# Optimization experiments

Hardware: AMD Instinct MI355X
Metric: run time of the kernel (lower is better)

Reference implementation:

```python
import jax, jax.numpy as jnp
import numpy as np

TOP_K = 2  # num_experts_per_tok


def setup_inputs() -> dict:
    key = jax.random.key(0)
    ks = jax.random.split(key, 5)
    B, T, D, E, F = 2, 2048, 1024, 8, 2048
    scale_d = 1.0 / np.sqrt(D)
    scale_f = 1.0 / np.sqrt(F)
    return {
        "x": jax.random.normal(ks[0], (B, T, D), jnp.float32),
        "kernel_router_DE": jax.random.normal(ks[1], (D, E), jnp.float32) * scale_d,
        "kernel_gating_EDF": jax.random.normal(ks[2], (E, D, F), jnp.float32) * scale_d,
        "kernel_up_EDF": jax.random.normal(ks[3], (E, D, F), jnp.float32) * scale_d,
        "kernel_down_EFD": jax.random.normal(ks[4], (E, F, D), jnp.float32) * scale_f,
    }


def reference(x, kernel_router_DE, kernel_gating_EDF, kernel_up_EDF, kernel_down_EFD):
    E = kernel_router_DE.shape[-1]
    x = x.astype(jnp.float32)

    # --- Router: logits -> softmax -> top_k -> renormalize with softmax ---
    router_logits_BTE = jnp.einsum('BTD,DE->BTE', x, kernel_router_DE)
    probs_BTE = jax.nn.softmax(router_logits_BTE.astype(jnp.float32), axis=-1)
    weights_BTX, indices_BTX = jax.lax.top_k(probs_BTE, TOP_K)
    norm_weights_BTX = jax.nn.softmax(weights_BTX, axis=-1)

    # --- Scatter top-k weights back to dense per-expert weights ---
    one_hot_BTXE = jax.nn.one_hot(indices_BTX, num_classes=E, dtype=jnp.float32)
    full_weights_BTE = jnp.sum(one_hot_BTXE * norm_weights_BTX[..., None], axis=2)

    # --- Dense all-expert MLP (gating * up -> down), weighted combine ---
    gating_BTEF = jnp.einsum('BTD,EDF->BTEF', x, kernel_gating_EDF)
    fuse_BTEF = jax.nn.silu(gating_BTEF) * jnp.einsum('BTD,EDF->BTEF', x, kernel_up_EDF)
    down_BTED = jnp.einsum('BTEF,EFD->BTED', fuse_BTEF, kernel_down_EFD)
    out_BTD = jnp.einsum('BTED,BTE->BTD', down_BTED, full_weights_BTE)
    return out_BTD.astype(jnp.float32)
```

## Files before the change

### kernel.cpp

```cpp
#include <hip/hip_runtime.h>
#include <cstdint>

#define N_TOK 4096
#define DIM   1024
#define NEXP  8
#define FDIM  2048

typedef _Float16 f16_t;
typedef _Float16 f16x8 __attribute__((ext_vector_type(8)));
typedef float    f32x4 __attribute__((ext_vector_type(4)));

__device__ inline unsigned packh(float a, float b) {
    union { f16_t h[2]; unsigned u; } p;
    p.h[0] = (f16_t)a; p.h[1] = (f16_t)b;
    return p.u;
}

__device__ inline void gl2lds16(const void* g, void* l) {
    __builtin_amdgcn_global_load_lds(
        (const __attribute__((address_space(1))) unsigned*)g,
        (__attribute__((address_space(3))) unsigned*)l, 16, 0, 0);
}

__device__ void transpose_tile(const float* __restrict__ in, f16_t* __restrict__ out,
                               int R, int C, int tiles_r, int tix, unsigned (*sP)[68])
{
    int rb = (tix % tiles_r) * 128;
    int cb = (tix / tiles_r) * 64;
    int t = threadIdx.x;
    int dp = t >> 2;
    int fc = (t & 3) * 16;
    const float* r0 = in + (size_t)(rb + 2 * dp) * C + cb + fc;
    const float* r1 = r0 + C;
#pragma unroll
    for (int j = 0; j < 16; j += 4) {
        float4 a = *(const float4*)(r0 + j);
        float4 b = *(const float4*)(r1 + j);
        sP[fc + j + 0][dp] = packh(a.x, b.x);
        sP[fc + j + 1][dp] = packh(a.y, b.y);
        sP[fc + j + 2][dp] = packh(a.z, b.z);
        sP[fc + j + 3][dp] = packh(a.w, b.w);
    }
    __syncthreads();
    int c = t >> 2;
    int rc = t & 3;
    uint4* dst = (uint4*)(out + (size_t)(cb + c) * R + rb + rc * 32);
    const unsigned* src = &sP[c][rc * 16];
#pragma unroll
    for (int j = 0; j < 4; j++)
        dst[j] = *(const uint4*)(src + j * 4);
}

__global__ __launch_bounds__(256) void prep_kernel(
    const float* __restrict__ x, const float* __restrict__ wr,
    const float* __restrict__ wg, const float* __restrict__ wu, const float* __restrict__ wd,
    f16_t* __restrict__ xf, f16_t* __restrict__ wgT, f16_t* __restrict__ wuT, f16_t* __restrict__ wdT,
    float* __restrict__ topw, int* __restrict__ counts, int* __restrict__ bucket)
{
    __shared__ union { float r[NEXP][DIM]; unsigned sP[64][68]; } sh;
    __shared__ int sIdx[32];
    int bx = blockIdx.x;
    int tid = threadIdx.x;

    if (bx >= 256) {
        if (bx < 256 + 4096) {
            int tix = bx - 256;
            int m = tix >> 8;
            int tt = tix & 255;
            const float* in = (m < 8) ? wg + (size_t)m * DIM * FDIM : wu + (size_t)(m - 8) * DIM * FDIM;
            f16_t* out      = (m < 8) ? wgT + (size_t)m * DIM * FDIM : wuT + (size_t)(m - 8) * DIM * FDIM;
            transpose_tile(in, out, DIM, FDIM, DIM / 128, tt, sh.sP);
        } else {
            int tix = bx - (256 + 4096);
            int m = tix >> 8;
            int tt = tix & 255;
            transpose_tile(wd + (size_t)m * FDIM * DIM, wdT + (size_t)m * FDIM * DIM,
                           FDIM, DIM, FDIM / 128, tt, sh.sP);
        }
        return;
    }

    for (int i = tid; i < DIM * NEXP / 4; i += 256) {
        float4 v = ((const float4*)wr)[i];
        int base = i * 4;
        sh.r[(base + 0) & 7][(base + 0) >> 3] = v.x;
        sh.r[(base + 1) & 7][(base + 1) >> 3] = v.y;
        sh.r[(base + 2) & 7][(base + 2) >> 3] = v.z;
        sh.r[(base + 3) & 7][(base + 3) >> 3] = v.w;
    }
    __syncthreads();
    int wave = tid >> 6, lane = tid & 63;
    int t0 = bx * 16 + wave * 4;
    for (int tt = 0; tt < 4; ++tt) {
        int t = t0 + tt;
        float acc[NEXP];
#pragma unroll
        for (int e = 0; e < NEXP; e++) acc[e] = 0.f;
        const float* xr = x + (size_t)t * DIM;
        f16_t* xo = xf + (size_t)t * DIM;
#pragma unroll
        for (int k = 0; k < DIM / 64; k++) {
            int d = lane + k * 64;
            float xv = xr[d];
            xo[d] = (f16_t)xv;
#pragma unroll
            for (int e = 0; e < NEXP; e++) acc[e] += xv * sh.r[e][d];
        }
#pragma unroll
        for (int e = 0; e < NEXP; e++) {
#pragma unroll
            for (int off = 32; off > 0; off >>= 1)
                acc[e] += __shfl_xor(acc[e], off, 64);
        }
        if (lane == 0) {
            float mx = acc[0];
#pragma unroll
            for (int e = 1; e < NEXP; e++) mx = fmaxf(mx, acc[e]);
            float p[NEXP]; float s = 0.f;
#pragma unroll
            for (int e = 0; e < NEXP; e++) { p[e] = expf(acc[e] - mx); s += p[e]; }
            float inv = 1.f / s;
#pragma unroll
            for (int e = 0; e < NEXP; e++) p[e] *= inv;
            int i1 = 0; float p1 = p[0];
#pragma unroll
            for (int e = 1; e < NEXP; e++) if (p[e] > p1) { p1 = p[e]; i1 = e; }
            int i2 = -1; float p2 = -1.f;
#pragma unroll
            for (int e = 0; e < NEXP; e++) if (e != i1 && p[e] > p2) { p2 = p[e]; i2 = e; }
            float e2 = expf(p2 - p1);
            float w1 = 1.f / (1.f + e2);
            topw[t * 2 + 0] = w1;
            topw[t * 2 + 1] = e2 * w1;
            int j = (wave * 4 + tt) * 2;
            sIdx[j + 0] = i1;
            sIdx[j + 1] = i2;
        }
    }
    __syncthreads();
    if (tid < NEXP) {
        int cnt = 0;
#pragma unroll
        for (int j = 0; j < 32; j++) cnt += (sIdx[j] == tid) ? 1 : 0;
        if (cnt > 0) {
            int pos = atomicAdd(&counts[tid * 32], cnt);
#pragma unroll
            for (int j = 0; j < 32; j++)
                if (sIdx[j] == tid)
                    bucket[tid * N_TOK + pos++] = (bx * 16 + (j >> 1)) * 2 + (j & 1);
        }
    }
}

__global__ __launch_bounds__(256) void transpose_d_kernel(
    const float* __restrict__ wd, f16_t* __restrict__ wdT)
{
    __shared__ unsigned sP[64][68];
    int m = blockIdx.x >> 8;
    int tt = blockIdx.x & 255;
    transpose_tile(wd + (size_t)m * FDIM * DIM, wdT + (size_t)m * FDIM * DIM,
                   FDIM, DIM, FDIM / 128, tt, sP);
}

__global__ __launch_bounds__(256) void gateup_kernel(
    const f16_t* __restrict__ xf,
    const f16_t* __restrict__ wgT, const f16_t* __restrict__ wuT,
    const int* __restrict__ counts, const int* __restrict__ bucket,
    const float* __restrict__ topw, f16_t* __restrict__ H)
{
    int e = blockIdx.z;
    int cnt = counts[e * 32];
    int m0 = blockIdx.y * 128;
    if (m0 >= cnt) return;
    int n0 = blockIdx.x * 64;

    __shared__ f16_t sA[128 * 32];
    __shared__ f16_t sBg[64 * 32];
    __shared__ f16_t sBu[64 * 32];
    __shared__ int sEnt[128];

    int tid = threadIdx.x;
    if (tid < 128) {
        int i = m0 + tid;
        sEnt[tid] = bucket[e * N_TOK + (i < cnt ? i : m0)];
    }
    __syncthreads();

    int wave = tid >> 6, lane = tid & 63;
    int q = ((lane & 3) - (lane >> 3)) & 3;
    int rA0 = wave * 32 + (lane >> 2);
    int rA1 = rA0 + 16;
    int rB  = wave * 16 + (lane >> 2);
    const f16_t* gA0 = xf + (size_t)(sEnt[rA0] >> 1) * DIM + q * 8;
    const f16_t* gA1 = xf + (size_t)(sEnt[rA1] >> 1) * DIM + q * 8;
    const f16_t* gBg = wgT + ((size_t)e * FDIM + n0 + rB) * DIM + q * 8;
    const f16_t* gBu = wuT + ((size_t)e * FDIM + n0 + rB) * DIM + q * 8;
    f16_t* lA0 = &sA[wave * 1024 + lane * 8];
    f16_t* lA1 = lA0 + 512;
    f16_t* lBg = &sBg[wave * 512 + lane * 8];
    f16_t* lBu = &sBu[wave * 512 + lane * 8];

    f32x4 accG[4][2], accU[4][2];
    f32x4 zero = {0.f, 0.f, 0.f, 0.f};
#pragma unroll
    for (int i = 0; i < 4; i++)
#pragma unroll
        for (int j = 0; j < 2; j++) { accG[i][j] = zero; accU[i][j] = zero; }

    int wm = (wave & 1) * 64, wn = (wave >> 1) * 32;
    int fm = lane & 15, quad = lane >> 4;
    int p8 = ((quad + (fm >> 1)) & 3) * 8;

    for (int k0 = 0; k0 < DIM; k0 += 32) {
        gl2lds16(gA0 + k0, lA0);
        gl2lds16(gA1 + k0, lA1);
        gl2lds16(gBg + k0, lBg);
        gl2lds16(gBu + k0, lBu);
        __syncthreads();
        f16x8 af[4], bg[2], bu[2];
#pragma unroll
        for (int mi = 0; mi < 4; mi++)
            af[mi] = *(const f16x8*)&sA[(wm + mi * 16 + fm) * 32 + p8];
#pragma unroll
        for (int ni = 0; ni < 2; ni++) {
            bg[ni] = *(const f16x8*)&sBg[(wn + ni * 16 + fm) * 32 + p8];
            bu[ni] = *(const f16x8*)&sBu[(wn + ni * 16 + fm) * 32 + p8];
        }
#pragma unroll
        for (int mi = 0; mi < 4; mi++)
#pragma unroll
            for (int ni = 0; ni < 2; ni++) {
                accG[mi][ni] = __builtin_amdgcn_mfma_f32_16x16x32_f16(af[mi], bg[ni], accG[mi][ni], 0, 0, 0);
                accU[mi][ni] = __builtin_amdgcn_mfma_f32_16x16x32_f16(af[mi], bu[ni], accU[mi][ni], 0, 0, 0);
            }
        __syncthreads();
    }
    int crow = quad * 4, ccol = fm;
#pragma unroll
    for (int mi = 0; mi < 4; mi++) {
#pragma unroll
        for (int i = 0; i < 4; i++) {
            int m = wm + mi * 16 + crow + i;
            if (m0 + m < cnt) {
                int ent = sEnt[m];
                float w = topw[ent];
                f16_t* hr = H + (size_t)ent * FDIM + n0 + wn;
#pragma unroll
                for (int ni = 0; ni < 2; ni++) {
                    float g = accG[mi][ni][i], u = accU[mi][ni][i];
                    float h = (g / (1.f + __expf(-g))) * u * w;
                    hr[ni * 16 + ccol] = (f16_t)h;
                }
            }
        }
    }
}

__global__ __launch_bounds__(256) void down_kernel(
    const f16_t* __restrict__ H, const f16_t* __restrict__ wdT,
    const int* __restrict__ counts, const int* __restrict__ bucket,
    float* __restrict__ Y)
{
    int e = blockIdx.z;
    int cnt = counts[e * 32];
    int m0 = blockIdx.y * 128;
    if (m0 >= cnt) return;
    int n0 = blockIdx.x * 128;

    __shared__ f16_t sA[128 * 32];
    __shared__ f16_t sB[128 * 32];
    __shared__ int sEnt[128];

    int tid = threadIdx.x;
    if (tid < 128) {
        int i = m0 + tid;
        sEnt[tid] = bucket[e * N_TOK + (i < cnt ? i : m0)];
    }
    __syncthreads();

    int wave = tid >> 6, lane = tid & 63;
    int q = ((lane & 3) - (lane >> 3)) & 3;
    int r0 = wave * 32 + (lane >> 2);
    int r1 = r0 + 16;
    const f16_t* gA0 = H + (size_t)sEnt[r0] * FDIM + q * 8;
    const f16_t* gA1 = H + (size_t)sEnt[r1] * FDIM + q * 8;
    const f16_t* gB0 = wdT + ((size_t)e * DIM + n0 + r0) * FDIM + q * 8;
    const f16_t* gB1 = wdT + ((size_t)e * DIM + n0 + r1) * FDIM + q * 8;
    f16_t* lA0 = &sA[wave * 1024 + lane * 8];
    f16_t* lA1 = lA0 + 512;
    f16_t* lB0 = &sB[wave * 1024 + lane * 8];
    f16_t* lB1 = lB0 + 512;

    f32x4 acc[4][4];
    f32x4 zero = {0.f, 0.f, 0.f, 0.f};
#pragma unroll
    for (int i = 0; i < 4; i++)
#pragma unroll
        for (int j = 0; j < 4; j++) acc[i][j] = zero;

    int wm = (wave & 1) * 64, wn = (wave >> 1) * 64;
    int fm = lane & 15, quad = lane >> 4;
    int p8 = ((quad + (fm >> 1)) & 3) * 8;

    for (int k0 = 0; k0 < FDIM; k0 += 32) {
        gl2lds16(gA0 + k0, lA0);
        gl2lds16(gA1 + k0, lA1);
        gl2lds16(gB0 + k0, lB0);
        gl2lds16(gB1 + k0, lB1);
        __syncthreads();
        f16x8 af[4], bf[4];
#pragma unroll
        for (int mi = 0; mi < 4; mi++)
            af[mi] = *(const f16x8*)&sA[(wm + mi * 16 + fm) * 32 + p8];
#pragma unroll
        for (int ni = 0; ni < 4; ni++)
            bf[ni] = *(const f16x8*)&sB[(wn + ni * 16 + fm) * 32 + p8];
#pragma unroll
        for (int mi = 0; mi < 4; mi++)
#pragma unroll
            for (int ni = 0; ni < 4; ni++)
                acc[mi][ni] = __builtin_amdgcn_mfma_f32_16x16x32_f16(af[mi], bf[ni], acc[mi][ni], 0, 0, 0);
        __syncthreads();
    }
    int crow = quad * 4, ccol = fm;
#pragma unroll
    for (int mi = 0; mi < 4; mi++) {
#pragma unroll
        for (int i = 0; i < 4; i++) {
            int m = wm + mi * 16 + crow + i;
            if (m0 + m < cnt) {
                int ent = sEnt[m];
                float* yr = Y + (size_t)ent * DIM + n0 + wn;
#pragma unroll
                for (int ni = 0; ni < 4; ni++)
                    yr[ni * 16 + ccol] = acc[mi][ni][i];
            }
        }
    }
}

__global__ __launch_bounds__(256) void combine_kernel(
    const float* __restrict__ Y, float* __restrict__ out)
{
    int i = blockIdx.x * 256 + threadIdx.x;
    int t = i >> 8;
    int c = i & 255;
    float4 a = ((const float4*)Y)[(size_t)(2 * t) * 256 + c];
    float4 b = ((const float4*)Y)[(size_t)(2 * t + 1) * 256 + c];
    float4 o;
    o.x = a.x + b.x; o.y = a.y + b.y; o.z = a.z + b.z; o.w = a.w + b.w;
    ((float4*)out)[i] = o;
}

extern "C" void kernel_launch(void* const* d_in, const int* in_sizes, int n_in,
                              void* d_out, int out_size, void* d_ws, size_t ws_size,
                              hipStream_t stream) {
    const float* x  = (const float*)d_in[0];
    const float* wr = (const float*)d_in[1];
    const float* wg = (const float*)d_in[2];
    const float* wu = (const float*)d_in[3];
    const float* wd = (const float*)d_in[4];
    float* out = (float*)d_out;
    char* ws = (char*)d_ws;
    const size_t MB = 1ull << 20;

    int*   counts = (int*)ws;
    int*   bucket = (int*)(ws + 1024);
    float* topw   = (float*)(ws + 160 * 1024);
    f16_t* xf     = (f16_t*)(ws + 1 * MB);
    f16_t* wgT    = (f16_t*)(ws + 9 * MB);
    f16_t* wuT    = (f16_t*)(ws + 41 * MB);
    f16_t* H      = (f16_t*)(ws + 73 * MB);

    bool big_ws = (ws_size >= 138 * MB);
    f16_t* wdT;
    float* Y;
    if (big_ws) {
        wdT = (f16_t*)(ws + 105 * MB);
        Y   = (float*)(ws + 1 * MB);
    } else {
        wdT = (f16_t*)(ws + 1 * MB);
        Y   = (float*)(ws + 33 * MB);
    }

    hipMemsetAsync(counts, 0, 1024, stream);
    int prep_blocks = 256 + 4096 + (big_ws ? 2048 : 0);
    prep_kernel<<<prep_blocks, 256, 0, stream>>>(x, wr, wg, wu, wd,
                                                 xf, wgT, wuT, wdT, topw, counts, bucket);
    gateup_kernel<<<dim3(FDIM / 64, 32, NEXP), 256, 0, stream>>>(xf, wgT, wuT, counts, bucket, topw, H);
    if (!big_ws)
        transpose_d_kernel<<<2048, 256, 0, stream>>>(wd, wdT);
    down_kernel<<<dim3(DIM / 128, 32, NEXP), 256, 0, stream>>>(H, wdT, counts, bucket, Y);
    combine_kernel<<<4096, 256, 0, stream>>>(Y, out);
}
```

Before: 447.9 us.

## Double K-tile depth to 64 in expert GEMMs and split prep kernel

Both grouped GEMM kernels (gate/up and down) now stage 64-wide K slices into LDS instead of 32, using an 8-way XOR-style swizzle, and issue two MFMAs per fragment per iteration. This halves the number of barrier pairs and loop iterations per tile, at the cost of doubling LDS use per block, which may lower occupancy. The fused prep kernel is split into separate router and gate/up transpose kernels. The large-workspace path is dropped, so the down-weight transpose now always runs as its own kernel before the down GEMM.

```diff
diff --git a/kernel.cpp b/kernel.cpp
--- a/kernel.cpp
+++ b/kernel.cpp
@@ -22,75 +22,25 @@
         (__attribute__((address_space(3))) unsigned*)l, 16, 0, 0);
 }
 
-__device__ void transpose_tile(const float* __restrict__ in, f16_t* __restrict__ out,
-                               int R, int C, int tiles_r, int tix, unsigned (*sP)[68])
-{
-    int rb = (tix % tiles_r) * 128;
-    int cb = (tix / tiles_r) * 64;
-    int t = threadIdx.x;
-    int dp = t >> 2;
-    int fc = (t & 3) * 16;
-    const float* r0 = in + (size_t)(rb + 2 * dp) * C + cb + fc;
-    const float* r1 = r0 + C;
-#pragma unroll
-    for (int j = 0; j < 16; j += 4) {
-        float4 a = *(const float4*)(r0 + j);
-        float4 b = *(const float4*)(r1 + j);
-        sP[fc + j + 0][dp] = packh(a.x, b.x);
-        sP[fc + j + 1][dp] = packh(a.y, b.y);
-        sP[fc + j + 2][dp] = packh(a.z, b.z);
-        sP[fc + j + 3][dp] = packh(a.w, b.w);
-    }
-    __syncthreads();
-    int c = t >> 2;
-    int rc = t & 3;
-    uint4* dst = (uint4*)(out + (size_t)(cb + c) * R + rb + rc * 32);
-    const unsigned* src = &sP[c][rc * 16];
-#pragma unroll
-    for (int j = 0; j < 4; j++)
-        dst[j] = *(const uint4*)(src + j * 4);
-}
-
-__global__ __launch_bounds__(256) void prep_kernel(
+__global__ __launch_bounds__(256) void router_kernel(
     const float* __restrict__ x, const float* __restrict__ wr,
-    const float* __restrict__ wg, const float* __restrict__ wu, const float* __restrict__ wd,
-    f16_t* __restrict__ xf, f16_t* __restrict__ wgT, f16_t* __restrict__ wuT, f16_t* __restrict__ wdT,
+    f16_t* __restrict__ xf,
     float* __restrict__ topw, int* __restrict__ counts, int* __restrict__ bucket)
 {
-    __shared__ union { float r[NEXP][DIM]; unsigned sP[64][68]; } sh;
+    __shared__ float r[NEXP][DIM];
     __shared__ int sIdx[32];
-    int bx = blockIdx.x;
     int tid = threadIdx.x;
-
-    if (bx >= 256) {
-        if (bx < 256 + 4096) {
-            int tix = bx - 256;
-            int m = tix >> 8;
-            int tt = tix & 255;
-            const float* in = (m < 8) ? wg + (size_t)m * DIM * FDIM : wu + (size_t)(m - 8) * DIM * FDIM;
-            f16_t* out      = (m < 8) ? wgT + (size_t)m * DIM * FDIM : wuT + (size_t)(m - 8) * DIM * FDIM;
-            transpose_tile(in, out, DIM, FDIM, DIM / 128, tt, sh.sP);
-        } else {
-            int tix = bx - (256 + 4096);
-            int m = tix >> 8;
-            int tt = tix & 255;
-            transpose_tile(wd + (size_t)m * FDIM * DIM, wdT + (size_t)m * FDIM * DIM,
-                           FDIM, DIM, FDIM / 128, tt, sh.sP);
-        }
-        return;
-    }
-
     for (int i = tid; i < DIM * NEXP / 4; i += 256) {
         float4 v = ((const float4*)wr)[i];
         int base = i * 4;
-        sh.r[(base + 0) & 7][(base + 0) >> 3] = v.x;
-        sh.r[(base + 1) & 7][(base + 1) >> 3] = v.y;
-        sh.r[(base + 2) & 7][(base + 2) >> 3] = v.z;
-        sh.r[(base + 3) & 7][(base + 3) >> 3] = v.w;
+        r[(base + 0) & 7][(base + 0) >> 3] = v.x;
+        r[(base + 1) & 7][(base + 1) >> 3] = v.y;
+        r[(base + 2) & 7][(base + 2) >> 3] = v.z;
+        r[(base + 3) & 7][(base + 3) >> 3] = v.w;
     }
     __syncthreads();
     int wave = tid >> 6, lane = tid & 63;
-    int t0 = bx * 16 + wave * 4;
+    int t0 = blockIdx.x * 16 + wave * 4;
     for (int tt = 0; tt < 4; ++tt) {
         int t = t0 + tt;
         float acc[NEXP];
@@ -104,7 +54,7 @@
             float xv = xr[d];
             xo[d] = (f16_t)xv;
 #pragma unroll
-            for (int e = 0; e < NEXP; e++) acc[e] += xv * sh.r[e][d];
+            for (int e = 0; e < NEXP; e++) acc[e] += xv * r[e][d];
         }
 #pragma unroll
         for (int e = 0; e < NEXP; e++) {
@@ -147,9 +97,50 @@
 #pragma unroll
             for (int j = 0; j < 32; j++)
                 if (sIdx[j] == tid)
-                    bucket[tid * N_TOK + pos++] = (bx * 16 + (j >> 1)) * 2 + (j & 1);
-        }
-    }
+                    bucket[tid * N_TOK + pos++] = (blockIdx.x * 16 + (j >> 1)) * 2 + (j & 1);
+        }
+    }
+}
+
+__device__ void transpose_tile(const float* __restrict__ in, f16_t* __restrict__ out,
+                               int R, int C, int tiles_r, int tix, unsigned (*sP)[68])
+{
+    int rb = (tix % tiles_r) * 128;
+    int cb = (tix / tiles_r) * 64;
+    int t = threadIdx.x;
+    int dp = t >> 2;
+    int fc = (t & 3) * 16;
+    const float* r0 = in + (size_t)(rb + 2 * dp) * C + cb + fc;
+    const float* r1 = r0 + C;
+#pragma unroll
+    for (int j = 0; j < 16; j += 4) {
+        float4 a = *(const float4*)(r0 + j);
+        float4 b = *(const float4*)(r1 + j);
+        sP[fc + j + 0][dp] = packh(a.x, b.x);
+        sP[fc + j + 1][dp] = packh(a.y, b.y);
+        sP[fc + j + 2][dp] = packh(a.z, b.z);
+        sP[fc + j + 3][dp] = packh(a.w, b.w);
+    }
+    __syncthreads();
+    int c = t >> 2;
+    int rc = t & 3;
+    uint4* dst = (uint4*)(out + (size_t)(cb + c) * R + rb + rc * 32);
+    const unsigned* src = &sP[c][rc * 16];
+#pragma unroll
+    for (int j = 0; j < 4; j++)
+        dst[j] = *(const uint4*)(src + j * 4);
+}
+
+__global__ __launch_bounds__(256) void transpose_gu_kernel(
+    const float* __restrict__ wg, const float* __restrict__ wu,
+    f16_t* __restrict__ wgT, f16_t* __restrict__ wuT)
+{
+    __shared__ unsigned sP[64][68];
+    int m = blockIdx.x >> 8;
+    int tt = blockIdx.x & 255;
+    const float* in = (m < 8) ? wg + (size_t)m * DIM * FDIM : wu + (size_t)(m - 8) * DIM * FDIM;
+    f16_t* out      = (m < 8) ? wgT + (size_t)m * DIM * FDIM : wuT + (size_t)(m - 8) * DIM * FDIM;
+    transpose_tile(in, out, DIM, FDIM, DIM / 128, tt, sP);
 }
 
 __global__ __launch_bounds__(256) void transpose_d_kernel(
@@ -174,9 +165,9 @@
     if (m0 >= cnt) return;
     int n0 = blockIdx.x * 64;
 
-    __shared__ f16_t sA[128 * 32];
-    __shared__ f16_t sBg[64 * 32];
-    __shared__ f16_t sBu[64 * 32];
+    __shared__ f16_t sA[128 * 64];
+    __shared__ f16_t sBg[64 * 64];
+    __shared__ f16_t sBu[64 * 64];
     __shared__ int sEnt[128];
 
     int tid = threadIdx.x;
@@ -187,18 +178,26 @@
     __syncthreads();
 
     int wave = tid >> 6, lane = tid & 63;
-    int q = ((lane & 3) - (lane >> 3)) & 3;
-    int rA0 = wave * 32 + (lane >> 2);
-    int rA1 = rA0 + 16;
-    int rB  = wave * 16 + (lane >> 2);
-    const f16_t* gA0 = xf + (size_t)(sEnt[rA0] >> 1) * DIM + q * 8;
-    const f16_t* gA1 = xf + (size_t)(sEnt[rA1] >> 1) * DIM + q * 8;
-    const f16_t* gBg = wgT + ((size_t)e * FDIM + n0 + rB) * DIM + q * 8;
-    const f16_t* gBu = wuT + ((size_t)e * FDIM + n0 + rB) * DIM + q * 8;
-    f16_t* lA0 = &sA[wave * 1024 + lane * 8];
-    f16_t* lA1 = lA0 + 512;
-    f16_t* lBg = &sBg[wave * 512 + lane * 8];
-    f16_t* lBu = &sBu[wave * 512 + lane * 8];
+    int sr = lane >> 3, p = lane & 7;
+
+    const f16_t* gA[4]; f16_t* lA[4];
+#pragma unroll
+    for (int j = 0; j < 4; j++) {
+        int r = wave * 32 + j * 8 + sr;
+        int g = (p - (r & 7)) & 7;
+        gA[j] = xf + (size_t)(sEnt[r] >> 1) * DIM + g * 8;
+        lA[j] = &sA[r * 64 + p * 8];
+    }
+    const f16_t *gBg[2], *gBu[2]; f16_t *lBg[2], *lBu[2];
+#pragma unroll
+    for (int j = 0; j < 2; j++) {
+        int r = wave * 16 + j * 8 + sr;
+        int g = (p - (r & 7)) & 7;
+        gBg[j] = wgT + ((size_t)e * FDIM + n0 + r) * DIM + g * 8;
+        gBu[j] = wuT + ((size_t)e * FDIM + n0 + r) * DIM + g * 8;
+        lBg[j] = &sBg[r * 64 + p * 8];
+        lBu[j] = &sBu[r * 64 + p * 8];
+    }
 
     f32x4 accG[4][2], accU[4][2];
     f32x4 zero = {0.f, 0.f, 0.f, 0.f};
@@ -209,29 +208,38 @@
 
     int wm = (wave & 1) * 64, wn = (wave >> 1) * 32;
     int fm = lane & 15, quad = lane >> 4;
-    int p8 = ((quad + (fm >> 1)) & 3) * 8;
-
-    for (int k0 = 0; k0 < DIM; k0 += 32) {
-        gl2lds16(gA0 + k0, lA0);
-        gl2lds16(gA1 + k0, lA1);
-        gl2lds16(gBg + k0, lBg);
-        gl2lds16(gBu + k0, lBu);
+    int p0 = ((quad + (fm & 7)) & 7) * 8;
+    int p1 = p0 ^ 32;
+
+    for (int k0 = 0; k0 < DIM; k0 += 64) {
+#pragma unroll
+        for (int j = 0; j < 4; j++) gl2lds16(gA[j] + k0, lA[j]);
+#pragma unroll
+        for (int j = 0; j < 2; j++) { gl2lds16(gBg[j] + k0, lBg[j]); gl2lds16(gBu[j] + k0, lBu[j]); }
         __syncthreads();
-        f16x8 af[4], bg[2], bu[2];
+        f16x8 a0[4], a1[4], bg0[2], bg1[2], bu0[2], bu1[2];
+#pragma unroll
+        for (int mi = 0; mi < 4; mi++) {
+            int row = (wm + mi * 16 + fm) * 64;
+            a0[mi] = *(const f16x8*)&sA[row + p0];
+            a1[mi] = *(const f16x8*)&sA[row + p1];
+        }
+#pragma unroll
+        for (int ni = 0; ni < 2; ni++) {
+            int row = (wn + ni * 16 + fm) * 64;
+            bg0[ni] = *(const f16x8*)&sBg[row + p0];
+            bg1[ni] = *(const f16x8*)&sBg[row + p1];
+            bu0[ni] = *(const f16x8*)&sBu[row + p0];
+            bu1[ni] = *(const f16x8*)&sBu[row + p1];
+        }
 #pragma unroll
         for (int mi = 0; mi < 4; mi++)
-            af[mi] = *(const f16x8*)&sA[(wm + mi * 16 + fm) * 32 + p8];
-#pragma unroll
-        for (int ni = 0; ni < 2; ni++) {
-            bg[ni] = *(const f16x8*)&sBg[(wn + ni * 16 + fm) * 32 + p8];
-            bu[ni] = *(const f16x8*)&sBu[(wn + ni * 16 + fm) * 32 + p8];
-        }
-#pragma unroll
-        for (int mi = 0; mi < 4; mi++)
 #pragma unroll
             for (int ni = 0; ni < 2; ni++) {
-                accG[mi][ni] = __builtin_amdgcn_mfma_f32_16x16x32_f16(af[mi], bg[ni], accG[mi][ni], 0, 0, 0);
-                accU[mi][ni] = __builtin_amdgcn_mfma_f32_16x16x32_f16(af[mi], bu[ni], accU[mi][ni], 0, 0, 0);
+                accG[mi][ni] = __builtin_amdgcn_mfma_f32_16x16x32_f16(a0[mi], bg0[ni], accG[mi][ni], 0, 0, 0);
+                accU[mi][ni] = __builtin_amdgcn_mfma_f32_16x16x32_f16(a0[mi], bu0[ni], accU[mi][ni], 0, 0, 0);
+                accG[mi][ni] = __builtin_amdgcn_mfma_f32_16x16x32_f16(a1[mi], bg1[ni], accG[mi][ni], 0, 0, 0);
+                accU[mi][ni] = __builtin_amdgcn_mfma_f32_16x16x32_f16(a1[mi], bu1[ni], accU[mi][ni], 0, 0, 0);
             }
         __syncthreads();
     }
@@ -267,8 +275,8 @@
     if (m0 >= cnt) return;
     int n0 = blockIdx.x * 128;
 
-    __shared__ f16_t sA[128 * 32];
-    __shared__ f16_t sB[128 * 32];
+    __shared__ f16_t sA[128 * 64];
+    __shared__ f16_t sB[128 * 64];
     __shared__ int sEnt[128];
 
     int tid = threadIdx.x;
@@ -279,17 +287,18 @@
     __syncthreads();
 
     int wave = tid >> 6, lane = tid & 63;
-    int q = ((lane & 3) - (lane >> 3)) & 3;
-    int r0 = wave * 32 + (lane >> 2);
-    int r1 = r0 + 16;
-    const f16_t* gA0 = H + (size_t)sEnt[r0] * FDIM + q * 8;
-    const f16_t* gA1 = H + (size_t)sEnt[r1] * FDIM + q * 8;
-    const f16_t* gB0 = wdT + ((size_t)e * DIM + n0 + r0) * FDIM + q * 8;
-    const f16_t* gB1 = wdT + ((size_t)e * DIM + n0 + r1) * FDIM + q * 8;
-    f16_t* lA0 = &sA[wave * 1024 + lane * 8];
-    f16_t* lA1 = lA0 + 512;
-    f16_t* lB0 = &sB[wave * 1024 + lane * 8];
-    f16_t* lB1 = lB0 + 512;
+    int sr = lane >> 3, p = lane & 7;
+
+    const f16_t *gA[4], *gB[4]; f16_t *lA[4], *lB[4];
+#pragma unroll
+    for (int j = 0; j < 4; j++) {
+        int r = wave * 32 + j * 8 + sr;
+        int g = (p - (r & 7)) & 7;
+        gA[j] = H + (size_t)sEnt[r] * FDIM + g * 8;
+        gB[j] = wdT + ((size_t)e * DIM + n0 + r) * FDIM + g * 8;
+        lA[j] = &sA[r * 64 + p * 8];
+        lB[j] = &sB[r * 64 + p * 8];
+    }
 
     f32x4 acc[4][4];
     f32x4 zero = {0.f, 0.f, 0.f, 0.f};
@@ -300,26 +309,33 @@
 
     int wm = (wave & 1) * 64, wn = (wave >> 1) * 64;
     int fm = lane & 15, quad = lane >> 4;
-    int p8 = ((quad + (fm >> 1)) & 3) * 8;
-
-    for (int k0 = 0; k0 < FDIM; k0 += 32) {
-        gl2lds16(gA0 + k0, lA0);
-        gl2lds16(gA1 + k0, lA1);
-        gl2lds16(gB0 + k0, lB0);
-        gl2lds16(gB1 + k0, lB1);
+    int p0 = ((quad + (fm & 7)) & 7) * 8;
+    int p1 = p0 ^ 32;
+
+    for (int k0 = 0; k0 < FDIM; k0 += 64) {
+#pragma unroll
+        for (int j = 0; j < 4; j++) { gl2lds16(gA[j] + k0, lA[j]); gl2lds16(gB[j] + k0, lB[j]); }
         __syncthreads();
-        f16x8 af[4], bf[4];
+        f16x8 a0[4], a1[4], b0[4], b1[4];
+#pragma unroll
+        for (int mi = 0; mi < 4; mi++) {
+            int row = (wm + mi * 16 + fm) * 64;
+            a0[mi] = *(const f16x8*)&sA[row + p0];
+            a1[mi] = *(const f16x8*)&sA[row + p1];
+        }
+#pragma unroll
+        for (int ni = 0; ni < 4; ni++) {
+            int row = (wn + ni * 16 + fm) * 64;
+            b0[ni] = *(const f16x8*)&sB[row + p0];
+            b1[ni] = *(const f16x8*)&sB[row + p1];
+        }
 #pragma unroll
         for (int mi = 0; mi < 4; mi++)
-            af[mi] = *(const f16x8*)&sA[(wm + mi * 16 + fm) * 32 + p8];
-#pragma unroll
-        for (int ni = 0; ni < 4; ni++)
-            bf[ni] = *(const f16x8*)&sB[(wn + ni * 16 + fm) * 32 + p8];
-#pragma unroll
-        for (int mi = 0; mi < 4; mi++)
-#pragma unroll
-            for (int ni = 0; ni < 4; ni++)
-                acc[mi][ni] = __builtin_amdgcn_mfma_f32_16x16x32_f16(af[mi], bf[ni], acc[mi][ni], 0, 0, 0);
+#pragma unroll
+            for (int ni = 0; ni < 4; ni++) {
+                acc[mi][ni] = __builtin_amdgcn_mfma_f32_16x16x32_f16(a0[mi], b0[ni], acc[mi][ni], 0, 0, 0);
+                acc[mi][ni] = __builtin_amdgcn_mfma_f32_16x16x32_f16(a1[mi], b1[ni], acc[mi][ni], 0, 0, 0);
+            }
         __syncthreads();
     }
     int crow = quad * 4, ccol = fm;
@@ -371,25 +387,14 @@
     f16_t* wgT    = (f16_t*)(ws + 9 * MB);
     f16_t* wuT    = (f16_t*)(ws + 41 * MB);
     f16_t* H      = (f16_t*)(ws + 73 * MB);
-
-    bool big_ws = (ws_size >= 138 * MB);
-    f16_t* wdT;
-    float* Y;
-    if (big_ws) {
-        wdT = (f16_t*)(ws + 105 * MB);
-        Y   = (float*)(ws + 1 * MB);
-    } else {
-        wdT = (f16_t*)(ws + 1 * MB);
-        Y   = (float*)(ws + 33 * MB);
-    }
+    f16_t* wdT    = (f16_t*)(ws + 1 * MB);
+    float* Y      = (float*)(ws + 33 * MB);
 
     hipMemsetAsync(counts, 0, 1024, stream);
-    int prep_blocks = 256 + 4096 + (big_ws ? 2048 : 0);
-    prep_kernel<<<prep_blocks, 256, 0, stream>>>(x, wr, wg, wu, wd,
-                                                 xf, wgT, wuT, wdT, topw, counts, bucket);
+    router_kernel<<<256, 256, 0, stream>>>(x, wr, xf, topw, counts, bucket);
+    transpose_gu_kernel<<<4096, 256, 0, stream>>>(wg, wu, wgT, wuT);
     gateup_kernel<<<dim3(FDIM / 64, 32, NEXP), 256, 0, stream>>>(xf, wgT, wuT, counts, bucket, topw, H);
-    if (!big_ws)
-        transpose_d_kernel<<<2048, 256, 0, stream>>>(wd, wdT);
+    transpose_d_kernel<<<2048, 256, 0, stream>>>(wd, wdT);
     down_kernel<<<dim3(DIM / 128, 32, NEXP), 256, 0, stream>>>(H, wdT, counts, bucket, Y);
     combine_kernel<<<4096, 256, 0, stream>>>(Y, out);
 }
```

Result: slower. 461.3 us (+3.0%).
